# Optimization experiments

Hardware: AMD Instinct MI355X
Metric: run time of the kernel (lower is better)

The kernel has to match this reference:

```python
import jax, jax.numpy as jnp
import numpy as np

BOUND = 1.0
N_RAYS = 2048
TOT = 128        # num_steps (samples per pixel)
IND_S = 16       # indicator_steps
MAX_DEPTHS = 2
HID = 64
EPS = 1e-8


def setup_inputs() -> dict:
    key = jax.random.key(0)
    ks = jax.random.split(key, 13)
    M = N_RAYS * TOT
    rays_o = 0.3 * jax.random.normal(ks[0], (N_RAYS, 3), jnp.float32)
    rd = jax.random.normal(ks[1], (N_RAYS, 3), jnp.float32)
    rays_d = rd / (jnp.linalg.norm(rd, axis=-1, keepdims=True) + EPS)
    env_map = 0.1 * jax.random.normal(ks[2], (3, 128, 256), jnp.float32)
    Wd1 = jax.random.normal(ks[3], (3, HID), jnp.float32) / np.sqrt(3.0)
    Wd2 = jax.random.normal(ks[4], (HID, 3), jnp.float32) / np.sqrt(HID)
    Wf1 = jax.random.normal(ks[5], (6, HID), jnp.float32) / np.sqrt(6.0)
    Ws = jax.random.normal(ks[6], (HID, 3), jnp.float32) / np.sqrt(HID)
    Wdir = jax.random.normal(ks[7], (HID, 3), jnp.float32) / np.sqrt(HID)
    Wrho = jax.random.normal(ks[8], (HID, 3), jnp.float32) / np.sqrt(HID)
    jitter = jax.random.uniform(ks[9], (MAX_DEPTHS, M, IND_S), jnp.float32)
    u_t = jax.random.uniform(ks[10], (MAX_DEPTHS, M), jnp.float32)
    u_scatter = jax.random.uniform(ks[11], (MAX_DEPTHS, M), jnp.float32)
    channel = jax.random.randint(ks[12], (MAX_DEPTHS, M), 0, 3)
    return dict(rays_o=rays_o, rays_d=rays_d, env_map=env_map, Wd1=Wd1, Wd2=Wd2,
                Wf1=Wf1, Ws=Ws, Wdir=Wdir, Wrho=Wrho,
                jitter=jitter, u_t=u_t, u_scatter=u_scatter, channel=channel)


def _density(pts, Wd1, Wd2):
    # stand-in NeRF density field: 3 spectral channels, positive
    return jax.nn.softplus(jnp.sin(pts @ Wd1) @ Wd2)


def _material(o, d, Wf1, Ws, Wdir, Wrho):
    f = jnp.tanh(jnp.concatenate([o, d], axis=-1) @ Wf1)
    sigma_t = jax.nn.softplus(f @ Ws)                     # [M,3]
    dn = f @ Wdir
    d_out = dn / (jnp.linalg.norm(dn, axis=-1, keepdims=True) + EPS)
    fused_rho = jax.nn.sigmoid(f @ Wrho)                  # [M,3]
    return sigma_t, d_out, fused_rho


def _sample_env(env_map, p):
    # equirectangular lookup == torch grid_sample(bilinear, align_corners=False, zero pad)
    x, y, z = p[:, 0], p[:, 1], p[:, 2]
    theta = jnp.nan_to_num(jnp.arctan2(x, -z)) / jnp.pi            # grid x in [-1,1]
    phi = 2.0 / jnp.pi * jnp.nan_to_num(jnp.arccos(y)) - 1.0       # grid y in [-1,1]
    C, H, W = env_map.shape
    ix = ((theta + 1.0) * W - 1.0) * 0.5
    iy = ((phi + 1.0) * H - 1.0) * 0.5
    x0 = jnp.floor(ix); y0 = jnp.floor(iy)
    wx = ix - x0; wy = iy - y0

    def tap(xc, yc, w):
        inb = (xc >= 0) & (xc < W) & (yc >= 0) & (yc < H)
        xi = jnp.clip(xc, 0, W - 1).astype(jnp.int32)
        yi = jnp.clip(yc, 0, H - 1).astype(jnp.int32)
        return (w * inb)[:, None] * env_map[:, yi, xi].T   # [M,3]

    v = (tap(x0, y0, (1 - wx) * (1 - wy)) + tap(x0 + 1, y0, wx * (1 - wy)) +
         tap(x0, y0 + 1, (1 - wx) * wy) + tap(x0 + 1, y0 + 1, wx * wy))
    return jnp.exp(v)


def _render(rays_o, rays_d, env_map, Wd1, Wd2, Wf1, Ws, Wdir, Wrho,
            jitter, u_t, u_scatter, channel):
    M = N_RAYS * TOT
    o = jnp.repeat(rays_o, TOT, axis=0)   # [M,3]
    d = jnp.repeat(rays_d, TOT, axis=0)
    alive = jnp.ones((M,), bool)          # masked version of boolean compaction
    thr = jnp.ones((M, 3), jnp.float32)
    rgbs = jnp.zeros((M, 3), jnp.float32)
    lin = jnp.linspace(0.0, 1.0, IND_S)

    for dep in range(MAX_DEPTHS):
        # ray-sphere intersection (radius=bound)
        a = jnp.sum(d * d, -1)
        b = 2.0 * jnp.sum(d * o, -1)
        c = jnp.sum(o * o, -1) - BOUND ** 2
        delta = b * b - 4.0 * a * c
        alive = alive & (delta > 0.0)
        sq = jnp.sqrt(jnp.maximum(delta, 0.0))
        nears = jnp.maximum((-b - sq) / (2.0 * a), 0.001)
        fars = jnp.maximum((-b + sq) / (2.0 * a), 0.001)
        span = fars - nears

        # stratified indicator samples -> per-channel majorant
        z = nears[:, None] + span[:, None] * lin[None, :]
        z = z + (jitter[dep] - 0.5) * (span[:, None] / IND_S)
        pts = o[:, None, :] + d[:, None, :] * z[:, :, None]          # [M,S,3]
        sigma = _density(pts.reshape(-1, 3), Wd1, Wd2).reshape(M, IND_S, 3)
        ch = channel[dep]
        maj_multi = jnp.maximum(sigma.max(axis=1), 0.001)            # [M,3]
        sig_ch = jnp.take_along_axis(sigma, ch[:, None, None], axis=2)[..., 0]
        maj = jnp.maximum(sig_ch.max(axis=1), 0.001)                 # [M]

        # free-flight sampling (last depth forces hit at far boundary)
        if dep < MAX_DEPTHS - 1:
            t = -jnp.log1p(-u_t[dep]) / maj + nears
        else:
            t = fars
        hit = alive & (t >= fars)

        # environment hit contribution
        denom = jnp.exp(-maj_multi * span[:, None]) / (maj_multi.max(-1, keepdims=True) + EPS) + EPS
        Le = _sample_env(env_map, o + d * fars[:, None])
        contrib = thr * (denom / jax.lax.stop_gradient(denom.mean(-1, keepdims=True))) * Le
        rgbs = rgbs + jnp.where(hit[:, None], contrib, 0.0)
        alive = alive & ~hit
        if dep == MAX_DEPTHS - 1:
            break

        # throughput update + null/real scattering (delta tracking)
        trans = jnp.exp(-maj_multi * (t - nears)[:, None]) / maj_multi.max(-1, keepdims=True)
        den2 = jax.lax.stop_gradient((maj_multi * trans).mean(-1, keepdims=True))
        thr = jnp.where(alive[:, None], thr * trans / den2, thr)
        o = jnp.where(alive[:, None], jax.lax.stop_gradient(o + d * t[:, None]), o)
        sigma_t, d_out, fused_rho = _material(o, d, Wf1, Ws, Wdir, Wrho)
        sp = jnp.minimum(jnp.take_along_axis(sigma_t, ch[:, None], axis=1)[:, 0] / maj, 1.0)
        sm = alive & (u_scatter[dep] < sp)
        d = jnp.where(sm[:, None], d_out, d)
        thr = jnp.where(sm[:, None], thr / (sp[:, None] + EPS) * fused_rho,
              jnp.where(alive[:, None], thr / (1.0 - sp[:, None] + EPS), thr))

    return rgbs.reshape(N_RAYS, TOT, 3).mean(axis=1)   # [N,3]


def reference(rays_o, rays_d, env_map, Wd1, Wd2, Wf1, Ws, Wdir, Wrho,
              jitter, u_t, u_scatter, channel):
    return _render(rays_o, rays_d, env_map, Wd1, Wd2, Wf1, Ws, Wdir, Wrho,
                   jitter, u_t, u_scatter, channel)
```

## Files before the change

kernel.cpp:

```cpp
#include <hip/hip_runtime.h>
#include <math.h>

#define NRAYS 2048
#define TOT   128
#define INDS  16
#define HID   64
#define EPSF  1e-8f
#define MTOT  (NRAYS*TOT)
#define NTAB  128

typedef float f32x2 __attribute__((ext_vector_type(2)));
typedef float f32x4 __attribute__((ext_vector_type(4)));

__device__ __forceinline__ float softplus_f(float x) {
    return fmaxf(x, 0.0f) + __logf(1.0f + __expf(-fabsf(x)));
}
__device__ __forceinline__ float sigmoid_f(float x) {
    return 1.0f / (1.0f + __expf(-x));
}
__device__ __forceinline__ float tanh_fast(float x) {
    float e2 = __expf(2.0f * x);
    return 1.0f - 2.0f / (e2 + 1.0f);
}
__device__ __forceinline__ f32x2 pkmax(f32x2 a, f32x2 b) {
    f32x2 r; r.x = fmaxf(a.x, b.x); r.y = fmaxf(a.y, b.y); return r;
}
__device__ __forceinline__ f32x2 pkfma(f32x2 a, f32x2 b, f32x2 c) {
    return __builtin_elementwise_fma(a, b, c);
}
__device__ __forceinline__ f32x4 fma4(f32x4 a, f32x4 b, f32x4 c) {
    return __builtin_elementwise_fma(a, b, c);
}

#define CK(i) ((float)(i)*(1.0f/15.0f) - 0.03125f)

#define MAKE_Z(jA, jB, kbase, nears, span)                                    \
    float s16 = (span) * (1.0f/16.0f);                                        \
    f32x2 z01, z23, z45, z67;                                                 \
    z01.x = fmaf((jA).x, s16, fmaf(span, CK((kbase)+0), nears));              \
    z01.y = fmaf((jA).y, s16, fmaf(span, CK((kbase)+1), nears));              \
    z23.x = fmaf((jA).z, s16, fmaf(span, CK((kbase)+2), nears));              \
    z23.y = fmaf((jA).w, s16, fmaf(span, CK((kbase)+3), nears));              \
    z45.x = fmaf((jB).x, s16, fmaf(span, CK((kbase)+4), nears));              \
    z45.y = fmaf((jB).y, s16, fmaf(span, CK((kbase)+5), nears));              \
    z67.x = fmaf((jB).z, s16, fmaf(span, CK((kbase)+6), nears));              \
    z67.y = fmaf((jB).w, s16, fmaf(span, CK((kbase)+7), nears));

#define DENSITY_J_BODY(A2, B2, W0, W1, W2v)                                   \
    {                                                                         \
        f32x2 g01 = pkfma(z01, (B2), (A2));                                   \
        f32x2 g23 = pkfma(z23, (B2), (A2));                                   \
        f32x2 g45 = pkfma(z45, (B2), (A2));                                   \
        f32x2 g67 = pkfma(z67, (B2), (A2));                                   \
        f32x2 h01, h23, h45, h67;                                             \
        h01.x = __builtin_amdgcn_sinf(g01.x); h01.y = __builtin_amdgcn_sinf(g01.y); \
        h23.x = __builtin_amdgcn_sinf(g23.x); h23.y = __builtin_amdgcn_sinf(g23.y); \
        h45.x = __builtin_amdgcn_sinf(g45.x); h45.y = __builtin_amdgcn_sinf(g45.y); \
        h67.x = __builtin_amdgcn_sinf(g67.x); h67.y = __builtin_amdgcn_sinf(g67.y); \
        a0_01 = pkfma(h01,(W0),a0_01); a0_23 = pkfma(h23,(W0),a0_23);         \
        a0_45 = pkfma(h45,(W0),a0_45); a0_67 = pkfma(h67,(W0),a0_67);         \
        a1_01 = pkfma(h01,(W1),a1_01); a1_23 = pkfma(h23,(W1),a1_23);         \
        a1_45 = pkfma(h45,(W1),a1_45); a1_67 = pkfma(h67,(W1),a1_67);         \
        a2_01 = pkfma(h01,(W2v),a2_01); a2_23 = pkfma(h23,(W2v),a2_23);       \
        a2_45 = pkfma(h45,(W2v),a2_45); a2_67 = pkfma(h67,(W2v),a2_67);       \
    }

__device__ __forceinline__ void density_max3_half_d1(
    const f32x4* __restrict__ sPW, const f32x4* __restrict__ sW01,
    const f32x2* __restrict__ sW2,
    float ox, float oy, float oz, float dx, float dy, float dz,
    float nears, float span, float4 jA, float4 jB, int kbase,
    float& mx0o, float& mx1o, float& mx2o)
{
    MAKE_Z(jA, jB, kbase, nears, span)
    f32x2 a0_01 = {0.f,0.f}, a0_23 = {0.f,0.f}, a0_45 = {0.f,0.f}, a0_67 = {0.f,0.f};
    f32x2 a1_01 = {0.f,0.f}, a1_23 = {0.f,0.f}, a1_45 = {0.f,0.f}, a1_67 = {0.f,0.f};
    f32x2 a2_01 = {0.f,0.f}, a2_23 = {0.f,0.f}, a2_45 = {0.f,0.f}, a2_67 = {0.f,0.f};
    #pragma unroll 2
    for (int j = 0; j < HID; ++j) {
        f32x4 pw  = sPW[j];
        f32x4 w01 = sW01[j];
        f32x2 w2  = sW2[j];
        float A = fmaf(ox, pw.x, fmaf(oy, pw.y, oz*pw.z));
        float B = fmaf(dx, pw.x, fmaf(dy, pw.y, dz*pw.z));
        f32x2 A2 = {A, A}, B2 = {B, B};
        f32x2 W0 = {w01.x, w01.y}, W1 = {w01.z, w01.w};
        DENSITY_J_BODY(A2, B2, W0, W1, w2)
    }
    f32x2 p0 = pkmax(pkmax(a0_01, a0_23), pkmax(a0_45, a0_67));
    f32x2 p1 = pkmax(pkmax(a1_01, a1_23), pkmax(a1_45, a1_67));
    f32x2 p2 = pkmax(pkmax(a2_01, a2_23), pkmax(a2_45, a2_67));
    mx0o = fmaxf(p0.x, p0.y);
    mx1o = fmaxf(p1.x, p1.y);
    mx2o = fmaxf(p2.x, p2.y);
}

__device__ __forceinline__ void env_logv(
    const float* __restrict__ env_map,
    float px, float py, float pz,
    float& v0, float& v1, float& v2)
{
    float theta = atan2f(px, -pz) * (1.0f/3.14159265358979323846f);
    float acv = (fabsf(py) <= 1.0f) ? acosf(py) : 0.0f;
    float phi = 0.63661977236758134308f * acv - 1.0f;
    float ixf = ((theta + 1.0f)*256.0f - 1.0f)*0.5f;
    float iyf = ((phi   + 1.0f)*128.0f - 1.0f)*0.5f;
    float x0f = floorf(ixf), y0f = floorf(iyf);
    float wx = ixf - x0f, wy = iyf - y0f;
    v0 = 0.f; v1 = 0.f; v2 = 0.f;
    auto tap = [&](float xc, float yc, float w) {
        if (xc >= 0.0f && xc < 256.0f && yc >= 0.0f && yc < 128.0f) {
            int xi = (int)xc, yi = (int)yc;
            const float* e = env_map + yi*256 + xi;
            v0 += w * e[0];
            v1 += w * e[128*256];
            v2 += w * e[2*128*256];
        }
    };
    tap(x0f,      y0f,      (1.0f-wx)*(1.0f-wy));
    tap(x0f+1.0f, y0f,      wx*(1.0f-wy));
    tap(x0f,      y0f+1.0f, (1.0f-wx)*wy);
    tap(x0f+1.0f, y0f+1.0f, wx*wy);
}

__global__ __launch_bounds__(256)
void render_kernel(const float* __restrict__ rays_o,
                   const float* __restrict__ rays_d,
                   const float* __restrict__ env_map,
                   const float* __restrict__ Wd1,
                   const float* __restrict__ Wd2,
                   const float* __restrict__ Wf1,
                   const float* __restrict__ Ws,
                   const float* __restrict__ Wdir,
                   const float* __restrict__ Wrho,
                   const float* __restrict__ jitter,
                   const float* __restrict__ u_t,
                   const float* __restrict__ u_scatter,
                   const int*   __restrict__ channel,
                   float* __restrict__ out)
{
    const int ray  = blockIdx.x;
    const int tid  = threadIdx.x;
    const int s    = tid >> 1;
    const int half = tid & 1;
    const int m    = ray * TOT + s;
    const int kbase = half * 8;

    __shared__ f32x4 sAB[HID];
    __shared__ f32x4 sW01[HID];
    __shared__ f32x2 sW2[HID];
    __shared__ f32x4 sPW[HID];
    __shared__ f32x4 sM0[HID];
    __shared__ f32x4 sM1[HID];
    __shared__ f32x4 sM2[HID];
    __shared__ f32x4 sTab[NTAB];
    __shared__ float sred[4][3];

    const float4* j0p = (const float4*)(jitter + (size_t)m*INDS + kbase);
    const float4* j1p = (const float4*)(jitter + ((size_t)MTOT + m)*INDS + kbase);
    float4 j0A = j0p[0], j0B = j0p[1];
    float4 j1A = j1p[0], j1B = j1p[1];
    int   ch = channel[m];
    float ut = u_t[m];
    float us = u_scatter[m];

    float ox = rays_o[ray*3+0], oy = rays_o[ray*3+1], oz = rays_o[ray*3+2];
    float dx = rays_d[ray*3+0], dy = rays_d[ray*3+1], dz = rays_d[ray*3+2];

    if (tid < HID) {
        const float INV2PI = 0.15915494309189535f;
        float w1x = Wd1[tid], w1y = Wd1[HID+tid], w1z = Wd1[2*HID+tid];
        float pw1x = w1x*INV2PI, pw1y = w1y*INV2PI, pw1z = w1z*INV2PI;
        float A = ox*pw1x + oy*pw1y + oz*pw1z;
        float B = dx*pw1x + dy*pw1y + dz*pw1z;
        float w20 = Wd2[3*tid], w21 = Wd2[3*tid+1], w22 = Wd2[3*tid+2];
        sAB[tid]  = (f32x4){A, A, B, B};
        sW01[tid] = (f32x4){w20, w20, w21, w21};
        sW2[tid]  = (f32x2){w22, w22};
        sPW[tid]  = (f32x4){pw1x, pw1y, pw1z, 0.0f};
        float f0 = Wf1[tid],       f1 = Wf1[HID+tid],   f2 = Wf1[2*HID+tid];
        float f3 = Wf1[3*HID+tid], f4 = Wf1[4*HID+tid], f5 = Wf1[5*HID+tid];
        float P = ox*f0 + oy*f1 + oz*f2 + dx*f3 + dy*f4 + dz*f5;
        float Q = dx*f0 + dy*f1 + dz*f2;
        sM0[tid] = (f32x4){P, Q, Ws[3*tid], Ws[3*tid+1]};
        sM1[tid] = (f32x4){Ws[3*tid+2], Wdir[3*tid], Wdir[3*tid+1], Wdir[3*tid+2]};
        sM2[tid] = (f32x4){Wrho[3*tid], Wrho[3*tid+1], Wrho[3*tid+2], 0.0f};
    }
    __syncthreads();

    float a0g = dx*dx + dy*dy + dz*dz;
    float b0g = 2.0f*(dx*ox + dy*oy + dz*oz);
    float c0g = (ox*ox + oy*oy + oz*oz) - 1.0f;
    float delta0 = b0g*b0g - 4.0f*a0g*c0g;
    bool alive = (delta0 > 0.0f);

    float nears = 0.f, fars = 0.f, span = 0.f, ztab0 = 0.f, invh = 0.f;
    if (alive) {
        float sq = sqrtf(delta0);
        nears = fmaxf((-b0g - sq) / (2.0f*a0g), 0.001f);
        fars  = fmaxf((-b0g + sq) / (2.0f*a0g), 0.001f);
        span  = fars - nears;
        ztab0 = fmaf(-span, 0.03125f, nears);
        float width = span * 1.0625f;
        float hstep = width * (1.0f/(NTAB-1));
        invh = (float)(NTAB-1) / width;
        int p = tid >> 1;
        float zp = fmaf((float)p, hstep, ztab0);
        float f0 = 0.f, f1 = 0.f, f2 = 0.f;
        const int jb = half * 32;
        #pragma unroll 4
        for (int j = jb; j < jb + 32; ++j) {
            f32x4 ab  = sAB[j];
            f32x4 w01 = sW01[j];
            f32x2 w2  = sW2[j];
            float hv = __builtin_amdgcn_sinf(fmaf(zp, ab.z, ab.x));
            f0 = fmaf(hv, w01.x, f0);
            f1 = fmaf(hv, w01.z, f1);
            f2 = fmaf(hv, w2.x, f2);
        }
        f0 += __shfl_xor(f0, 1, 64);
        f1 += __shfl_xor(f1, 1, 64);
        f2 += __shfl_xor(f2, 1, 64);
        if (half == 0) sTab[p] = (f32x4){f0, f1, f2, 0.0f};
    }
    __syncthreads();

    float thr0 = 1.f, thr1 = 1.f, thr2 = 1.f;
    float rgb0 = 0.f, rgb1 = 0.f, rgb2 = 0.f;

    if (alive) {
        MAKE_Z(j0A, j0B, kbase, nears, span)
        float mx0 = -1e30f, mx1 = -1e30f, mx2 = -1e30f;
#define TAB_EVAL(zz)                                                          \
        {                                                                     \
            float x = (zz - ztab0) * invh;                                    \
            x = fminf(fmaxf(x, 0.0f), (float)(NTAB-1) - 1e-3f);               \
            int i = (int)x; float w = x - (float)i;                           \
            f32x4 Ta = sTab[i]; f32x4 Tb = sTab[i+1];                         \
            f32x4 wv = {w, w, w, w};                                          \
            f32x4 F = fma4(wv, Tb - Ta, Ta);                                  \
            mx0 = fmaxf(mx0, F.x); mx1 = fmaxf(mx1, F.y); mx2 = fmaxf(mx2, F.z); \
        }
        TAB_EVAL(z01.x) TAB_EVAL(z01.y) TAB_EVAL(z23.x) TAB_EVAL(z23.y)
        TAB_EVAL(z45.x) TAB_EVAL(z45.y) TAB_EVAL(z67.x) TAB_EVAL(z67.y)
#undef TAB_EVAL
        mx0 = fmaxf(mx0, __shfl_xor(mx0, 1, 64));
        mx1 = fmaxf(mx1, __shfl_xor(mx1, 1, 64));
        mx2 = fmaxf(mx2, __shfl_xor(mx2, 1, 64));

        float maj0 = fmaxf(softplus_f(mx0), 0.001f);
        float maj1 = fmaxf(softplus_f(mx1), 0.001f);
        float maj2 = fmaxf(softplus_f(mx2), 0.001f);
        float mmax = fmaxf(fmaxf(maj0, maj1), maj2);

        float maj = (ch == 0) ? maj0 : ((ch == 1) ? maj1 : maj2);
        float t   = -log1pf(-ut) / maj + nears;

        if (t >= fars) {
            float den0 = __expf(-maj0*span)/(mmax+EPSF) + EPSF;
            float den1 = __expf(-maj1*span)/(mmax+EPSF) + EPSF;
            float den2 = __expf(-maj2*span)/(mmax+EPSF) + EPSF;
            float idm = 3.0f / (den0+den1+den2);
            float v0,v1,v2;
            env_logv(env_map, fmaf(dx,fars,ox), fmaf(dy,fars,oy), fmaf(dz,fars,oz), v0,v1,v2);
            rgb0 = den0*idm*__expf(v0);
            rgb1 = den1*idm*__expf(v1);
            rgb2 = den2*idm*__expf(v2);
            alive = false;
        } else {
            float tn  = t - nears;
            float imm = 1.0f / mmax;
            float tr0 = __expf(-maj0*tn) * imm;
            float tr1 = __expf(-maj1*tn) * imm;
            float tr2 = __expf(-maj2*tn) * imm;
            float i2m = 3.0f / (maj0*tr0 + maj1*tr1 + maj2*tr2);
            thr0 = tr0 * i2m;
            thr1 = tr1 * i2m;
            thr2 = tr2 * i2m;
            ox = fmaf(dx, t, ox); oy = fmaf(dy, t, oy); oz = fmaf(dz, t, oz);

            float st0=0.f, st1=0.f, st2=0.f;
            float dn0=0.f, dn1=0.f, dn2v=0.f;
            float rh0=0.f, rh1=0.f, rh2=0.f;
            const int j0 = half * 32;
            #pragma unroll 2
            for (int j = j0; j < j0 + 32; ++j) {
                f32x4 q0 = sM0[j];
                f32x4 q1 = sM1[j];
                f32x4 q2 = sM2[j];
                float pre = fmaf(t, q0.y, q0.x);
                float f = tanh_fast(pre);
                st0  = fmaf(f, q0.z, st0);
                st1  = fmaf(f, q0.w, st1);
                st2  = fmaf(f, q1.x, st2);
                dn0  = fmaf(f, q1.y, dn0);
                dn1  = fmaf(f, q1.z, dn1);
                dn2v = fmaf(f, q1.w, dn2v);
                rh0  = fmaf(f, q2.x, rh0);
                rh1  = fmaf(f, q2.y, rh1);
                rh2  = fmaf(f, q2.z, rh2);
            }
            st0  += __shfl_xor(st0, 1, 64);
            st1  += __shfl_xor(st1, 1, 64);
            st2  += __shfl_xor(st2, 1, 64);
            dn0  += __shfl_xor(dn0, 1, 64);
            dn1  += __shfl_xor(dn1, 1, 64);
            dn2v += __shfl_xor(dn2v, 1, 64);
            rh0  += __shfl_xor(rh0, 1, 64);
            rh1  += __shfl_xor(rh1, 1, 64);
            rh2  += __shfl_xor(rh2, 1, 64);

            float stch = (ch == 0) ? st0 : ((ch == 1) ? st1 : st2);
            float sp = fminf(softplus_f(stch) / maj, 1.0f);
            if (us < sp) {
                float inr = 1.0f / (sqrtf(dn0*dn0 + dn1*dn1 + dn2v*dn2v) + EPSF);
                dx = dn0*inr; dy = dn1*inr; dz = dn2v*inr;
                float isp = 1.0f/(sp + EPSF);
                thr0 *= isp * sigmoid_f(rh0);
                thr1 *= isp * sigmoid_f(rh1);
                thr2 *= isp * sigmoid_f(rh2);
            } else {
                float iv = 1.0f/(1.0f - sp + EPSF);
                thr0 *= iv; thr1 *= iv; thr2 *= iv;
            }
        }
    }

    if (alive) {
        float a = dx*dx + dy*dy + dz*dz;
        float b = 2.0f*(dx*ox + dy*oy + dz*oz);
        float c = (ox*ox + oy*oy + oz*oz) - 1.0f;
        float delta = b*b - 4.0f*a*c;
        if (delta > 0.0f) {
            float sq     = sqrtf(delta);
            float nears1 = fmaxf((-b - sq) / (2.0f*a), 0.001f);
            float fars1  = fmaxf((-b + sq) / (2.0f*a), 0.001f);
            float span1  = fars1 - nears1;

            float mx0, mx1, mx2;
            density_max3_half_d1(sPW, sW01, sW2, ox,oy,oz, dx,dy,dz, nears1, span1,
                                 j1A, j1B, kbase, mx0,mx1,mx2);
            mx0 = fmaxf(mx0, __shfl_xor(mx0, 1, 64));
            mx1 = fmaxf(mx1, __shfl_xor(mx1, 1, 64));
            mx2 = fmaxf(mx2, __shfl_xor(mx2, 1, 64));

            float maj0 = fmaxf(softplus_f(mx0), 0.001f);
            float maj1 = fmaxf(softplus_f(mx1), 0.001f);
            float maj2 = fmaxf(softplus_f(mx2), 0.001f);
            float mmax = fmaxf(fmaxf(maj0, maj1), maj2);

            float den0 = __expf(-maj0*span1)/(mmax+EPSF) + EPSF;
            float den1 = __expf(-maj1*span1)/(mmax+EPSF) + EPSF;
            float den2 = __expf(-maj2*span1)/(mmax+EPSF) + EPSF;
            float idm = 3.0f / (den0+den1+den2);
            float v0,v1,v2;
            env_logv(env_map, fmaf(dx,fars1,ox), fmaf(dy,fars1,oy), fmaf(dz,fars1,oz), v0,v1,v2);
            rgb0 += thr0 * den0*idm*__expf(v0);
            rgb1 += thr1 * den1*idm*__expf(v1);
            rgb2 += thr2 * den2*idm*__expf(v2);
        }
    }

    float r0 = rgb0, r1 = rgb1, r2 = rgb2;
    #pragma unroll
    for (int off = 32; off > 0; off >>= 1) {
        r0 += __shfl_down(r0, off, 64);
        r1 += __shfl_down(r1, off, 64);
        r2 += __shfl_down(r2, off, 64);
    }
    int wave = tid >> 6;
    if ((tid & 63) == 0) {
        sred[wave][0] = r0; sred[wave][1] = r1; sred[wave][2] = r2;
    }
    __syncthreads();
    if (tid == 0) {
        out[ray*3+0] = (sred[0][0]+sred[1][0]+sred[2][0]+sred[3][0]) * (1.0f/256.0f);
        out[ray*3+1] = (sred[0][1]+sred[1][1]+sred[2][1]+sred[3][1]) * (1.0f/256.0f);
        out[ray*3+2] = (sred[0][2]+sred[1][2]+sred[2][2]+sred[3][2]) * (1.0f/256.0f);
    }
}

extern "C" void kernel_launch(void* const* d_in, const int* in_sizes, int n_in,
                              void* d_out, int out_size, void* d_ws, size_t ws_size,
                              hipStream_t stream) {
    const float* rays_o    = (const float*)d_in[0];
    const float* rays_d    = (const float*)d_in[1];
    const float* env_map   = (const float*)d_in[2];
    const float* Wd1       = (const float*)d_in[3];
    const float* Wd2       = (const float*)d_in[4];
    const float* Wf1       = (const float*)d_in[5];
    const float* Ws        = (const float*)d_in[6];
    const float* Wdir      = (const float*)d_in[7];
    const float* Wrho      = (const float*)d_in[8];
    const float* jitter    = (const float*)d_in[9];
    const float* u_t       = (const float*)d_in[10];
    const float* u_scatter = (const float*)d_in[11];
    const int*   channel   = (const int*)d_in[12];
    float* out = (float*)d_out;

    render_kernel<<<dim3(NRAYS), dim3(256), 0, stream>>>(
        rays_o, rays_d, env_map, Wd1, Wd2, Wf1, Ws, Wdir, Wrho,
        jitter, u_t, u_scatter, channel, out);
}
```

Baseline: 168.5 us.

## Compact scattered rays into shared pool and reuse table for null-scatter depth-1

Rays that real-scatter at depth 0 are compacted into a shared-memory pool via an atomic counter and then evaluated densely by contiguous thread pairs, which is meant to remove divergence in the expensive depth-1 density MLP. Null-scatter rays keep their direction, so their depth-1 majorant is looked up in the precomputed per-ray density table at offset positions instead of being recomputed. The environment lookup for an unchanged direction is done once per block and shared. This adds a block barrier, atomics and shared-memory staging. It also relies on the same-ray geometry matching the table range, so samples outside that range get clamped, and the env reuse assumes the exit point maps to the same texel.

```diff
diff --git a/kernel.cpp b/kernel.cpp
--- a/kernel.cpp
+++ b/kernel.cpp
@@ -45,6 +45,17 @@
     z45.y = fmaf((jB).y, s16, fmaf(span, CK((kbase)+5), nears));              \
     z67.x = fmaf((jB).z, s16, fmaf(span, CK((kbase)+6), nears));              \
     z67.y = fmaf((jB).w, s16, fmaf(span, CK((kbase)+7), nears));
+
+#define TAB_EVAL(zz, mx0, mx1, mx2)                                           \
+    {                                                                         \
+        float x = ((zz) - ztab0) * invh;                                      \
+        x = fminf(fmaxf(x, 0.0f), (float)(NTAB-1) - 1e-3f);                   \
+        int i = (int)x; float w = x - (float)i;                               \
+        f32x4 Ta = sTab[i]; f32x4 Tb = sTab[i+1];                             \
+        f32x4 wv = {w, w, w, w};                                              \
+        f32x4 F = fma4(wv, Tb - Ta, Ta);                                      \
+        mx0 = fmaxf(mx0, F.x); mx1 = fmaxf(mx1, F.y); mx2 = fmaxf(mx2, F.z);  \
+    }
 
 #define DENSITY_J_BODY(A2, B2, W0, W1, W2v)                                   \
     {                                                                         \
@@ -154,6 +165,11 @@
     __shared__ f32x4 sM1[HID];
     __shared__ f32x4 sM2[HID];
     __shared__ f32x4 sTab[NTAB];
+    __shared__ f32x4 sP0[TOT];
+    __shared__ f32x4 sP1[TOT];
+    __shared__ f32x2 sP2[TOT];
+    __shared__ float sEnvE[3];
+    __shared__ int   sCnt;
     __shared__ float sred[4][3];
 
     const float4* j0p = (const float4*)(jitter + (size_t)m*INDS + kbase);
@@ -167,6 +183,7 @@
     float ox = rays_o[ray*3+0], oy = rays_o[ray*3+1], oz = rays_o[ray*3+2];
     float dx = rays_d[ray*3+0], dy = rays_d[ray*3+1], dz = rays_d[ray*3+2];
 
+    if (tid == 0) sCnt = 0;
     if (tid < HID) {
         const float INV2PI = 0.15915494309189535f;
         float w1x = Wd1[tid], w1y = Wd1[HID+tid], w1z = Wd1[2*HID+tid];
@@ -222,28 +239,27 @@
         f1 += __shfl_xor(f1, 1, 64);
         f2 += __shfl_xor(f2, 1, 64);
         if (half == 0) sTab[p] = (f32x4){f0, f1, f2, 0.0f};
+        if (tid == 0) {
+            float v0,v1,v2;
+            env_logv(env_map, fmaf(dx,fars,ox), fmaf(dy,fars,oy), fmaf(dz,fars,oz),
+                     v0,v1,v2);
+            sEnvE[0] = __expf(v0); sEnvE[1] = __expf(v1); sEnvE[2] = __expf(v2);
+        }
     }
     __syncthreads();
 
     float thr0 = 1.f, thr1 = 1.f, thr2 = 1.f;
     float rgb0 = 0.f, rgb1 = 0.f, rgb2 = 0.f;
+    bool  tab_d1 = false;
+    float tadv = 0.f;
 
     if (alive) {
         MAKE_Z(j0A, j0B, kbase, nears, span)
         float mx0 = -1e30f, mx1 = -1e30f, mx2 = -1e30f;
-#define TAB_EVAL(zz)                                                          \
-        {                                                                     \
-            float x = (zz - ztab0) * invh;                                    \
-            x = fminf(fmaxf(x, 0.0f), (float)(NTAB-1) - 1e-3f);               \
-            int i = (int)x; float w = x - (float)i;                           \
-            f32x4 Ta = sTab[i]; f32x4 Tb = sTab[i+1];                         \
-            f32x4 wv = {w, w, w, w};                                          \
-            f32x4 F = fma4(wv, Tb - Ta, Ta);                                  \
-            mx0 = fmaxf(mx0, F.x); mx1 = fmaxf(mx1, F.y); mx2 = fmaxf(mx2, F.z); \
-        }
-        TAB_EVAL(z01.x) TAB_EVAL(z01.y) TAB_EVAL(z23.x) TAB_EVAL(z23.y)
-        TAB_EVAL(z45.x) TAB_EVAL(z45.y) TAB_EVAL(z67.x) TAB_EVAL(z67.y)
-#undef TAB_EVAL
+        TAB_EVAL(z01.x, mx0,mx1,mx2) TAB_EVAL(z01.y, mx0,mx1,mx2)
+        TAB_EVAL(z23.x, mx0,mx1,mx2) TAB_EVAL(z23.y, mx0,mx1,mx2)
+        TAB_EVAL(z45.x, mx0,mx1,mx2) TAB_EVAL(z45.y, mx0,mx1,mx2)
+        TAB_EVAL(z67.x, mx0,mx1,mx2) TAB_EVAL(z67.y, mx0,mx1,mx2)
         mx0 = fmaxf(mx0, __shfl_xor(mx0, 1, 64));
         mx1 = fmaxf(mx1, __shfl_xor(mx1, 1, 64));
         mx2 = fmaxf(mx2, __shfl_xor(mx2, 1, 64));
@@ -261,12 +277,9 @@
             float den1 = __expf(-maj1*span)/(mmax+EPSF) + EPSF;
             float den2 = __expf(-maj2*span)/(mmax+EPSF) + EPSF;
             float idm = 3.0f / (den0+den1+den2);
-            float v0,v1,v2;
-            env_logv(env_map, fmaf(dx,fars,ox), fmaf(dy,fars,oy), fmaf(dz,fars,oz), v0,v1,v2);
-            rgb0 = den0*idm*__expf(v0);
-            rgb1 = den1*idm*__expf(v1);
-            rgb2 = den2*idm*__expf(v2);
-            alive = false;
+            rgb0 = den0*idm*sEnvE[0];
+            rgb1 = den1*idm*sEnvE[1];
+            rgb2 = den2*idm*sEnvE[2];
         } else {
             float tn  = t - nears;
             float imm = 1.0f / mmax;
@@ -314,32 +327,44 @@
             float sp = fminf(softplus_f(stch) / maj, 1.0f);
             if (us < sp) {
                 float inr = 1.0f / (sqrtf(dn0*dn0 + dn1*dn1 + dn2v*dn2v) + EPSF);
-                dx = dn0*inr; dy = dn1*inr; dz = dn2v*inr;
+                float ndx = dn0*inr, ndy = dn1*inr, ndz = dn2v*inr;
                 float isp = 1.0f/(sp + EPSF);
-                thr0 *= isp * sigmoid_f(rh0);
-                thr1 *= isp * sigmoid_f(rh1);
-                thr2 *= isp * sigmoid_f(rh2);
+                float t0 = thr0 * isp * sigmoid_f(rh0);
+                float t1 = thr1 * isp * sigmoid_f(rh1);
+                float t2 = thr2 * isp * sigmoid_f(rh2);
+                if (half == 0) {
+                    int sl = atomicAdd(&sCnt, 1);
+                    sP0[sl] = (f32x4){ox, oy, oz, ndx};
+                    sP1[sl] = (f32x4){ndy, ndz, t0, t1};
+                    sP2[sl] = (f32x2){t2, (float)m};
+                }
             } else {
                 float iv = 1.0f/(1.0f - sp + EPSF);
                 thr0 *= iv; thr1 *= iv; thr2 *= iv;
+                tab_d1 = true;
+                tadv = t;
             }
         }
     }
-
-    if (alive) {
-        float a = dx*dx + dy*dy + dz*dz;
-        float b = 2.0f*(dx*ox + dy*oy + dz*oz);
-        float c = (ox*ox + oy*oy + oz*oz) - 1.0f;
-        float delta = b*b - 4.0f*a*c;
-        if (delta > 0.0f) {
-            float sq     = sqrtf(delta);
-            float nears1 = fmaxf((-b - sq) / (2.0f*a), 0.001f);
-            float fars1  = fmaxf((-b + sq) / (2.0f*a), 0.001f);
+    __syncthreads();
+    int npool = sCnt;
+
+    if (tab_d1) {
+        float a1 = dx*dx + dy*dy + dz*dz;
+        float b1 = 2.0f*(dx*ox + dy*oy + dz*oz);
+        float c1 = (ox*ox + oy*oy + oz*oz) - 1.0f;
+        float delta1 = b1*b1 - 4.0f*a1*c1;
+        if (delta1 > 0.0f) {
+            float sq1    = sqrtf(delta1);
+            float nears1 = fmaxf((-b1 - sq1) / (2.0f*a1), 0.001f);
+            float fars1  = fmaxf((-b1 + sq1) / (2.0f*a1), 0.001f);
             float span1  = fars1 - nears1;
-
-            float mx0, mx1, mx2;
-            density_max3_half_d1(sPW, sW01, sW2, ox,oy,oz, dx,dy,dz, nears1, span1,
-                                 j1A, j1B, kbase, mx0,mx1,mx2);
+            MAKE_Z(j1A, j1B, kbase, nears1, span1)
+            float mx0 = -1e30f, mx1 = -1e30f, mx2 = -1e30f;
+            TAB_EVAL(tadv + z01.x, mx0,mx1,mx2) TAB_EVAL(tadv + z01.y, mx0,mx1,mx2)
+            TAB_EVAL(tadv + z23.x, mx0,mx1,mx2) TAB_EVAL(tadv + z23.y, mx0,mx1,mx2)
+            TAB_EVAL(tadv + z45.x, mx0,mx1,mx2) TAB_EVAL(tadv + z45.y, mx0,mx1,mx2)
+            TAB_EVAL(tadv + z67.x, mx0,mx1,mx2) TAB_EVAL(tadv + z67.y, mx0,mx1,mx2)
             mx0 = fmaxf(mx0, __shfl_xor(mx0, 1, 64));
             mx1 = fmaxf(mx1, __shfl_xor(mx1, 1, 64));
             mx2 = fmaxf(mx2, __shfl_xor(mx2, 1, 64));
@@ -353,11 +378,58 @@
             float den1 = __expf(-maj1*span1)/(mmax+EPSF) + EPSF;
             float den2 = __expf(-maj2*span1)/(mmax+EPSF) + EPSF;
             float idm = 3.0f / (den0+den1+den2);
-            float v0,v1,v2;
-            env_logv(env_map, fmaf(dx,fars1,ox), fmaf(dy,fars1,oy), fmaf(dz,fars1,oz), v0,v1,v2);
-            rgb0 += thr0 * den0*idm*__expf(v0);
-            rgb1 += thr1 * den1*idm*__expf(v1);
-            rgb2 += thr2 * den2*idm*__expf(v2);
+            rgb0 += thr0 * den0*idm*sEnvE[0];
+            rgb1 += thr1 * den1*idm*sEnvE[1];
+            rgb2 += thr2 * den2*idm*sEnvE[2];
+        }
+    }
+
+    {
+        int q = tid >> 1;
+        if (q < npool) {
+            f32x4 p0 = sP0[q];
+            f32x4 p1 = sP1[q];
+            f32x2 p2 = sP2[q];
+            float pox = p0.x, poy = p0.y, poz = p0.z;
+            float pdx = p0.w, pdy = p1.x, pdz = p1.y;
+            float pt0 = p1.z, pt1 = p1.w, pt2 = p2.x;
+            int   mm  = (int)p2.y;
+            const float4* jp = (const float4*)(jitter + ((size_t)MTOT + mm)*INDS + kbase);
+            float4 jA = jp[0], jB = jp[1];
+
+            float a1 = pdx*pdx + pdy*pdy + pdz*pdz;
+            float b1 = 2.0f*(pdx*pox + pdy*poy + pdz*poz);
+            float c1 = (pox*pox + poy*poy + poz*poz) - 1.0f;
+            float delta1 = b1*b1 - 4.0f*a1*c1;
+            if (delta1 > 0.0f) {
+                float sq1    = sqrtf(delta1);
+                float nears1 = fmaxf((-b1 - sq1) / (2.0f*a1), 0.001f);
+                float fars1  = fmaxf((-b1 + sq1) / (2.0f*a1), 0.001f);
+                float span1  = fars1 - nears1;
+
+                float mx0, mx1, mx2;
+                density_max3_half_d1(sPW, sW01, sW2, pox,poy,poz, pdx,pdy,pdz,
+                                     nears1, span1, jA, jB, kbase, mx0,mx1,mx2);
+                mx0 = fmaxf(mx0, __shfl_xor(mx0, 1, 64));
+                mx1 = fmaxf(mx1, __shfl_xor(mx1, 1, 64));
+                mx2 = fmaxf(mx2, __shfl_xor(mx2, 1, 64));
+
+                float maj0 = fmaxf(softplus_f(mx0), 0.001f);
+                float maj1 = fmaxf(softplus_f(mx1), 0.001f);
+                float maj2 = fmaxf(softplus_f(mx2), 0.001f);
+                float mmax = fmaxf(fmaxf(maj0, maj1), maj2);
+
+                float den0 = __expf(-maj0*span1)/(mmax+EPSF) + EPSF;
+                float den1 = __expf(-maj1*span1)/(mmax+EPSF) + EPSF;
+                float den2 = __expf(-maj2*span1)/(mmax+EPSF) + EPSF;
+                float idm = 3.0f / (den0+den1+den2);
+                float v0,v1,v2;
+                env_logv(env_map, fmaf(pdx,fars1,pox), fmaf(pdy,fars1,poy),
+                         fmaf(pdz,fars1,poz), v0,v1,v2);
+                rgb0 += pt0 * den0*idm*__expf(v0);
+                rgb1 += pt1 * den1*idm*__expf(v1);
+                rgb2 += pt2 * den2*idm*__expf(v2);
+            }
         }
     }
 
```

New measurement: 168.1 us. About the same (-0.3%).
